# Kernel optimization log

Measured on AMD Instinct MI355X. Metric: run time of the kernel, lower is better.

Reference implementation:

```python
import jax, jax.numpy as jnp
import numpy as np

B, S, HID, NH, NKV, HD, PS = 4, 1024, 4096, 32, 8, 128, 16
PPS = S // PS            # pages per sequence
NP = B * PPS             # total pages
NNZ = B * S


def _llama31_freqs(head_dim):
    # flashinfer apply_llama31_rope defaults: theta=5e5, scale=8, low=1, high=4, old_ctx=8192
    half = head_dim // 2
    theta, scale, low_ff, high_ff, old_ctx = 500000.0, 8.0, 1.0, 4.0, 8192.0
    freq = 1.0 / (theta ** (jnp.arange(half, dtype=jnp.float32) * 2.0 / head_dim))
    wavelen = 2.0 * jnp.pi / freq
    low_wl, high_wl = old_ctx / low_ff, old_ctx / high_ff
    smooth = (old_ctx / wavelen - low_ff) / (high_ff - low_ff)
    return jnp.where(wavelen < high_wl, freq,
                     jnp.where(wavelen > low_wl, freq / scale,
                               (1.0 - smooth) * freq / scale + smooth * freq))


def _rope(x, pos, freqs):
    # x: [nnz, H, D], non-interleaved (rotate-half) layout
    ang = pos.astype(jnp.float32)[:, None] * freqs[None, :]          # [nnz, D/2]
    cos, sin = jnp.cos(ang)[:, None, :], jnp.sin(ang)[:, None, :]    # [nnz, 1, D/2]
    x1, x2 = jnp.split(x, 2, axis=-1)
    return jnp.concatenate([x1 * cos - x2 * sin, x2 * cos + x1 * sin], axis=-1)


def setup_inputs() -> dict:
    key = jax.random.key(0)
    ks = jax.random.split(key, 6)
    std = 0.02
    return {
        "hidden_states": jax.random.normal(ks[0], (NNZ, HID), jnp.float32),
        "wq": jax.random.normal(ks[1], (NH * HD, HID), jnp.float32) * std,
        "wk": jax.random.normal(ks[2], (NKV * HD, HID), jnp.float32) * std,
        "wv": jax.random.normal(ks[3], (NKV * HD, HID), jnp.float32) * std,
        "wo": jax.random.normal(ks[4], (HID, NH * HD), jnp.float32) * std,
        "kv_cache": jnp.zeros((1, NP, 2, PS, NKV, HD), jnp.float32),
        "position_ids": jnp.tile(jnp.arange(S, dtype=jnp.int32), B),
        "kv_page_indices": jnp.arange(NP, dtype=jnp.int32),
        "kv_page_indptr": jnp.arange(B + 1, dtype=jnp.int32) * PPS,
        "kv_last_page_lens": jnp.full((B,), PS, jnp.int32),
        "qo_indptr": jnp.arange(B + 1, dtype=jnp.int32) * S,
    }


def reference(hidden_states, wq, wk, wv, wo, kv_cache, position_ids,
              kv_page_indices, kv_page_indptr, kv_last_page_lens, qo_indptr):
    nnz = hidden_states.shape[0]
    b = qo_indptr.shape[0] - 1
    s = nnz // b
    # fused QKV projections (nn.Linear stores [out, in])
    q = (hidden_states @ wq.T).reshape(nnz, NH, HD)
    k = (hidden_states @ wk.T).reshape(nnz, NKV, HD)
    v = (hidden_states @ wv.T).reshape(nnz, NKV, HD)
    # inline Llama-3.1 RoPE with per-token position ids
    freqs = _llama31_freqs(HD)
    q = _rope(q, position_ids, freqs)
    k = _rope(k, position_ids, freqs)
    # paged-KV append: scatter k/v into pages at (page_id, slot)
    cache = kv_cache[0]                                   # [NP, 2, PS, NKV, HD]
    ps = cache.shape[2]
    pages = kv_page_indices.reshape(b, -1)                # [B, PPS]
    bidx = jnp.repeat(jnp.arange(b), s)
    pid = pages[bidx, position_ids // ps]
    slot = position_ids % ps
    cache = cache.at[pid, 0, slot].set(k).at[pid, 1, slot].set(v)
    # paged attention: gather per-sequence K/V from pages, causal SDPA with GQA
    flat = pages.reshape(-1)
    kf = cache[flat, 0].reshape(b, s, NKV, HD)
    vf = cache[flat, 1].reshape(b, s, NKV, HD)
    g = NH // NKV
    kr = jnp.repeat(kf, g, axis=2)                        # [B, S, NH, HD]
    vr = jnp.repeat(vf, g, axis=2)
    qb = q.reshape(b, s, NH, HD)
    scale = 1.0 / jnp.sqrt(jnp.float32(HD))
    scores = jnp.einsum('bqhd,bkhd->bhqk', qb, kr) * scale
    mask = jnp.tril(jnp.ones((s, s), bool))
    scores = jnp.where(mask[None, None], scores, jnp.float32(-1e30))
    attn = jax.nn.softmax(scores, axis=-1)
    out = jnp.einsum('bhqk,bkhd->bqhd', attn, vr).reshape(nnz, NH * HD)
    return out @ wo.T
```

## Files before the change

kernel.cpp:

```cpp
#include <hip/hip_runtime.h>

typedef unsigned short u16;
typedef __bf16 bf16x8 __attribute__((ext_vector_type(8)));
typedef float f32x4 __attribute__((ext_vector_type(4)));

__device__ __forceinline__ u16 f2bf(float f) {
  unsigned int u = __float_as_uint(f);
  u += 0x7fffu + ((u >> 16) & 1u);
  return (u16)(u >> 16);
}
__device__ __forceinline__ float bf2f(u16 v) {
  return __uint_as_float(((unsigned int)v) << 16);
}

__device__ __forceinline__ void gl_lds16(const u16* g, u16* l) {
  auto* lp = reinterpret_cast<__attribute__((address_space(3))) unsigned int*>(
      reinterpret_cast<uintptr_t>(l));
  auto* gp = reinterpret_cast<const __attribute__((address_space(1))) unsigned int*>(
      reinterpret_cast<uintptr_t>(g));
  __builtin_amdgcn_global_load_lds(gp, lp, 16, 0, 0);
}

__global__ __launch_bounds__(256) void cvt_kernel(const float* __restrict__ in,
                                                  u16* __restrict__ out, int n4) {
  int i = blockIdx.x * 256 + threadIdx.x;
  if (i >= n4) return;
  float4 v = ((const float4*)in)[i];
  ushort4 o;
  o.x = f2bf(v.x); o.y = f2bf(v.y); o.z = f2bf(v.z); o.w = f2bf(v.w);
  ((ushort4*)out)[i] = o;
}


#define BARRIER() __builtin_amdgcn_s_barrier()
#define VMCNT(n_) asm volatile("s_waitcnt vmcnt(" #n_ ")" ::: "memory")
#define PH_SYNC()                                           \
  do {                                                      \
    BARRIER();                                              \
    asm volatile("s_waitcnt lgkmcnt(0)" ::: "memory");      \
    __builtin_amdgcn_sched_barrier(0);                      \
  } while (0)

#define STAGE_A(b_, h_, kt_)                                                        \
  gl_lds16(gA + (size_t)((h_) * 128) * K + (size_t)(kt_) * 32,                      \
           lds + (b_) * 16384 + (h_) * 4096 + w * 512)

#define STAGE_B(b_, h_, kt_)                                                        \
  gl_lds16(gB + (size_t)((h_) * 128) * K + (size_t)(kt_) * 32,                      \
           lds + (b_) * 16384 + 8192 + (h_) * 4096 + w * 512)

#define LOADS_A(b_, qm_)                                                            \
  do {                                                                              \
    _Pragma("unroll") for (int i2 = 0; i2 < 4; i2++)                                \
      ar[i2] = *(const bf16x8*)&lds[(b_) * 16384 + arow + ((qm_)*4 + i2) * 512 + ax]; \
  } while (0)

#define LOADS_B(b_, qn_)                                                            \
  do {                                                                              \
    _Pragma("unroll") for (int j2 = 0; j2 < 2; j2++)                                \
      br[(qn_)*2 + j2] =                                                            \
          *(const bf16x8*)&lds[(b_) * 16384 + brow + ((qn_)*2 + j2) * 512 + ax];    \
  } while (0)

#define MFMA_Q(qm_, qn_)                                                            \
  do {                                                                              \
    __builtin_amdgcn_s_setprio(1);                                                  \
    _Pragma("unroll") for (int i2 = 0; i2 < 4; i2++) {                              \
      _Pragma("unroll") for (int j2 = 0; j2 < 2; j2++) {                            \
        acc[(qm_)*4 + i2][(qn_)*2 + j2] = __builtin_amdgcn_mfma_f32_16x16x32_bf16(  \
            ar[i2], br[(qn_)*2 + j2], acc[(qm_)*4 + i2][(qn_)*2 + j2], 0, 0, 0);    \
      }                                                                             \
    }                                                                               \
    __builtin_amdgcn_s_setprio(0);                                                  \
  } while (0)

template <int OUT_BF16>
__global__ __launch_bounds__(512, 2) void gemm8p(const u16* __restrict__ A,
                                                 const u16* __restrict__ B,
                                                 void* __restrict__ Cv,
                                                 int M, int N, int K) {
  __shared__ u16 lds[32768];
  (void)M;
  const int t = threadIdx.x, lane = t & 63, w = t >> 6;
  const int col = lane & 15, quad = lane >> 4;
  const int wm = w >> 2, wn = w & 3;

  const int nwg = gridDim.x * gridDim.y;
  const int wgid = blockIdx.y * gridDim.x + blockIdx.x;
  const int xcd = wgid & 7, lin = wgid >> 3;
  const int q8 = nwg >> 3, r8 = nwg & 7;
  const int nid = (xcd < r8 ? xcd * (q8 + 1) : r8 * (q8 + 1) + (xcd - r8) * q8) + lin;
  const int m0 = (nid / gridDim.x) * 256;
  const int n0 = (nid % gridDim.x) * 256;

  const int pr_ = t >> 3;
  const int s_ = (t & 7) ^ (pr_ & 7);
  const int srow = (pr_ << 1) | (s_ >> 2);
  const int sj = s_ & 3;
  const u16* gA = A + (size_t)(m0 + srow) * K + sj * 8;
  const u16* gB = B + (size_t)(n0 + srow) * K + sj * 8;

  const int arow = wm * 4096;
  const int brow = 8192 + wn * 2048;
  const int ax = (col >> 1) * 64 +
                 (((((col & 1) << 2) | quad) ^ (col >> 1)) << 3);

  f32x4 acc[8][4] = {};
  bf16x8 ar[4], br[4];

  STAGE_A(0, 0, 0); STAGE_A(0, 1, 0);
  STAGE_B(0, 0, 0); STAGE_B(0, 1, 0);
  STAGE_B(1, 0, 1); STAGE_B(1, 1, 1);
  VMCNT(2);
  BARRIER();

  const int NIT = K >> 6;
  for (int it = 0; it < NIT - 1; ++it) {
    const int kt = it * 2;
    LOADS_A(0, 0); LOADS_B(0, 0);
    STAGE_A(1, 0, kt + 1);
    PH_SYNC(); MFMA_Q(0, 0); BARRIER();
    LOADS_B(0, 1);
    STAGE_A(1, 1, kt + 1);
    PH_SYNC(); MFMA_Q(0, 1); BARRIER();
    LOADS_A(0, 1);
    STAGE_B(0, 0, kt + 2);
    PH_SYNC(); MFMA_Q(1, 0); BARRIER();
    STAGE_B(0, 1, kt + 2);
    PH_SYNC(); MFMA_Q(1, 1); VMCNT(2); BARRIER();
    LOADS_A(1, 0); LOADS_B(1, 0);
    STAGE_A(0, 0, kt + 2);
    PH_SYNC(); MFMA_Q(0, 0); BARRIER();
    LOADS_B(1, 1);
    STAGE_A(0, 1, kt + 2);
    PH_SYNC(); MFMA_Q(0, 1); BARRIER();
    LOADS_A(1, 1);
    STAGE_B(1, 0, kt + 3);
    PH_SYNC(); MFMA_Q(1, 0); BARRIER();
    STAGE_B(1, 1, kt + 3);
    PH_SYNC(); MFMA_Q(1, 1); VMCNT(2); BARRIER();
  }

  {
    const int kl = 2 * NIT - 1;
    LOADS_A(0, 0); LOADS_B(0, 0);
    STAGE_A(1, 0, kl);
    PH_SYNC(); MFMA_Q(0, 0); BARRIER();
    LOADS_B(0, 1);
    STAGE_A(1, 1, kl);
    PH_SYNC(); MFMA_Q(0, 1); BARRIER();
    LOADS_A(0, 1);
    PH_SYNC(); MFMA_Q(1, 0); BARRIER();
    PH_SYNC(); MFMA_Q(1, 1); VMCNT(0); BARRIER();
    LOADS_A(1, 0); LOADS_B(1, 0);
    PH_SYNC(); MFMA_Q(0, 0); BARRIER();
    LOADS_B(1, 1);
    PH_SYNC(); MFMA_Q(0, 1); BARRIER();
    LOADS_A(1, 1);
    PH_SYNC(); MFMA_Q(1, 0); BARRIER();
    MFMA_Q(1, 1);
  }

#pragma unroll
  for (int i = 0; i < 8; i++) {
#pragma unroll
    for (int j = 0; j < 4; j++) {
      const int mb = m0 + wm * 128 + i * 16 + quad * 4;
      const int n = n0 + wn * 64 + j * 16 + col;
#pragma unroll
      for (int r = 0; r < 4; r++) {
        float v = acc[i][j][r];
        if constexpr (OUT_BF16)
          ((u16*)Cv)[(size_t)(mb + r) * N + n] = f2bf(v);
        else
          ((float*)Cv)[(size_t)(mb + r) * N + n] = v;
      }
    }
  }
}

__global__ __launch_bounds__(256) void transpose_kernel(const u16* __restrict__ in,
                                                        u16* __restrict__ out,
                                                        int in_stride, int out_stride) {
  __shared__ u16 tile[64][72];
  const int t = threadIdx.x;
  const int bm = blockIdx.y;
  const int bn = blockIdx.x;
  const int r = t >> 3, c = (t & 7) * 8;
  const u16* src = in + (size_t)(bm * 64 + r) * in_stride + bn * 64 + c;
  *(uint4*)&tile[r][c] = *(const uint4*)src;
  *(uint4*)&tile[r + 32][c] = *(const uint4*)(src + (size_t)32 * in_stride);
  __syncthreads();
  u16 vals[8];
  u16* dst = out + (size_t)(bn * 64 + r) * out_stride + bm * 64 + c;
#pragma unroll
  for (int i = 0; i < 8; i++) vals[i] = tile[c + i][r];
  *(uint4*)dst = *(uint4*)vals;
#pragma unroll
  for (int i = 0; i < 8; i++) vals[i] = tile[c + i][r + 32];
  *(uint4*)(dst + (size_t)32 * out_stride) = *(uint4*)vals;
}

__global__ __launch_bounds__(256) void rope_kernel(u16* __restrict__ X,
                                                   const int* __restrict__ pos_ids,
                                                   int log2H, int row_stride) {
  int tid = blockIdx.x * 256 + threadIdx.x;
  int i = tid & 63;
  int rest = tid >> 6;
  int h = rest & ((1 << log2H) - 1);
  int token = rest >> log2H;
  float pos = (float)pos_ids[token];
  float fr = __builtin_exp2f(-(float)i * (18.93156856932417f / 64.0f));
  float wl = 6.283185307179586f / fr;
  float f2;
  if (wl < 2048.0f) f2 = fr;
  else if (wl > 8192.0f) f2 = fr * 0.125f;
  else {
    float sm = (8192.0f / wl - 1.0f) * (1.0f / 3.0f);
    f2 = (1.0f - sm) * fr * 0.125f + sm * fr;
  }
  float ang = pos * f2;
  float ss = sinf(ang), cc = cosf(ang);
  size_t base = (size_t)token * row_stride + (size_t)h * 128 + i;
  float x1 = bf2f(X[base]), x2 = bf2f(X[base + 64]);
  X[base] = f2bf(x1 * cc - x2 * ss);
  X[base + 64] = f2bf(x2 * cc + x1 * ss);
}

__global__ __launch_bounds__(256) void attn_kernel(const u16* __restrict__ Qg,
                                                   const u16* __restrict__ Kg,
                                                   const u16* __restrict__ VTg,
                                                   u16* __restrict__ Og,
                                                   int QS, int KS) {
  const int qt = 15 - blockIdx.x;
  const int h = blockIdx.y, b = blockIdx.z;
  const int kvh = h >> 2;
  const int t = threadIdx.x, lane = t & 63, w = t >> 6;
  const int col = lane & 15, quad = lane >> 4;

  __shared__ u16 Ks[64 * 128];
  __shared__ u16 Vt[128 * 64];
  __shared__ u16 Ps[4][16][72];

  {
    const u16* Qbase = Qg + (size_t)(b * 1024 + qt * 64) * QS + h * 128;
#pragma unroll
    for (int c = 0; c < 4; c++) {
      int ch = w * 4 + c;
      int row = ch * 4 + (lane >> 4);
      int g = (lane & 15) ^ (row & 15);
      gl_lds16(Qbase + (size_t)row * QS + g * 8, Ks + ch * 512);
    }
  }
  __syncthreads();
  bf16x8 qa[4];
#pragma unroll
  for (int kk = 0; kk < 4; kk++) {
    int row = w * 16 + col;
    qa[kk] = *(const bf16x8*)&Ks[row * 128 + (((quad + 4 * kk) ^ col) << 3)];
  }

  f32x4 o[8] = {};
  float m_i[4] = {-3.0e38f, -3.0e38f, -3.0e38f, -3.0e38f};
  float l_i[4] = {};

  const float cf = 0.08838834764831845f * 1.4426950408889634f;
  const int qrow0 = qt * 64 + w * 16 + quad * 4;

  const u16* Kbase = Kg + (size_t)(b * 1024) * KS + kvh * 128;
  const u16* Vbase = VTg + (size_t)(kvh * 128) * 4096 + b * 1024;

  for (int j = 0; j <= qt; j++) {
    __syncthreads();
#pragma unroll
    for (int c = 0; c < 4; c++) {
      int ch = w * 4 + c;
      int krow = ch * 4 + (lane >> 4);
      int kg = (lane & 15) ^ (krow & 15);
      gl_lds16(Kbase + (size_t)(j * 64 + krow) * KS + kg * 8, Ks + ch * 512);
      int vrow = ch * 8 + (lane >> 3);
      int vg = (lane & 7) ^ (vrow & 7);
      gl_lds16(Vbase + (size_t)vrow * 4096 + j * 64 + vg * 8, Vt + ch * 512);
    }
    __syncthreads();

    f32x4 s[4] = {};
#pragma unroll
    for (int nb = 0; nb < 4; nb++) {
      int key = nb * 16 + col;
#pragma unroll
      for (int kk = 0; kk < 4; kk++) {
        bf16x8 kb2 = *(const bf16x8*)&Ks[key * 128 + (((quad + 4 * kk) ^ col) << 3)];
        s[nb] = __builtin_amdgcn_mfma_f32_16x16x32_bf16(qa[kk], kb2, s[nb], 0, 0, 0);
      }
    }

    if (j == qt) {
#pragma unroll
      for (int nb = 0; nb < 4; nb++)
#pragma unroll
        for (int rr = 0; rr < 4; rr++)
          if (j * 64 + nb * 16 + col > qrow0 + rr) s[nb][rr] = -3.0e38f;
    }

    float mnew[4];
#pragma unroll
    for (int rr = 0; rr < 4; rr++) {
      mnew[rr] = m_i[rr];
#pragma unroll
      for (int nb = 0; nb < 4; nb++) mnew[rr] = fmaxf(mnew[rr], s[nb][rr]);
    }
#pragma unroll
    for (int off = 1; off < 16; off <<= 1)
#pragma unroll
      for (int rr = 0; rr < 4; rr++)
        mnew[rr] = fmaxf(mnew[rr], __shfl_xor(mnew[rr], off));

    float p[4][4], rs[4], alpha[4];
#pragma unroll
    for (int rr = 0; rr < 4; rr++) {
      alpha[rr] = __builtin_exp2f((m_i[rr] - mnew[rr]) * cf);
      m_i[rr] = mnew[rr];
      rs[rr] = 0.0f;
    }
#pragma unroll
    for (int nb = 0; nb < 4; nb++)
#pragma unroll
      for (int rr = 0; rr < 4; rr++) {
        p[nb][rr] = __builtin_exp2f((s[nb][rr] - mnew[rr]) * cf);
        rs[rr] += p[nb][rr];
      }
#pragma unroll
    for (int off = 1; off < 16; off <<= 1)
#pragma unroll
      for (int rr = 0; rr < 4; rr++) rs[rr] += __shfl_xor(rs[rr], off);
#pragma unroll
    for (int rr = 0; rr < 4; rr++) l_i[rr] = l_i[rr] * alpha[rr] + rs[rr];
#pragma unroll
    for (int nb2 = 0; nb2 < 8; nb2++)
#pragma unroll
      for (int rr = 0; rr < 4; rr++) o[nb2][rr] *= alpha[rr];

#pragma unroll
    for (int nb = 0; nb < 4; nb++)
#pragma unroll
      for (int rr = 0; rr < 4; rr++)
        Ps[w][quad * 4 + rr][nb * 16 + col] = f2bf(p[nb][rr]);

    bf16x8 pa0 = *(const bf16x8*)&Ps[w][col][quad * 8];
    bf16x8 pa1 = *(const bf16x8*)&Ps[w][col][quad * 8 + 32];
#pragma unroll
    for (int nb2 = 0; nb2 < 8; nb2++) {
      int d = nb2 * 16 + col;
      bf16x8 vb0 = *(const bf16x8*)&Vt[d * 64 + ((quad ^ (col & 7)) << 3)];
      bf16x8 vb1 = *(const bf16x8*)&Vt[d * 64 + ((((quad + 4) & 7) ^ (col & 7)) << 3)];
      o[nb2] = __builtin_amdgcn_mfma_f32_16x16x32_bf16(pa0, vb0, o[nb2], 0, 0, 0);
      o[nb2] = __builtin_amdgcn_mfma_f32_16x16x32_bf16(pa1, vb1, o[nb2], 0, 0, 0);
    }
  }

  float inv[4];
#pragma unroll
  for (int rr = 0; rr < 4; rr++) inv[rr] = 1.0f / l_i[rr];
#pragma unroll
  for (int nb2 = 0; nb2 < 8; nb2++)
#pragma unroll
    for (int rr = 0; rr < 4; rr++) {
      size_t off2 = (size_t)(b * 1024 + qt * 64 + w * 16 + quad * 4 + rr) * 4096 +
                    h * 128 + nb2 * 16 + col;
      Og[off2] = f2bf(o[nb2][rr] * inv[rr]);
    }
}

extern "C" void kernel_launch(void* const* d_in, const int* in_sizes, int n_in,
                              void* d_out, int out_size, void* d_ws, size_t ws_size,
                              hipStream_t stream) {
  const float* hs = (const float*)d_in[0];
  const float* wq = (const float*)d_in[1];
  const float* wk = (const float*)d_in[2];
  const float* wv = (const float*)d_in[3];
  const float* wo = (const float*)d_in[4];
  const int* pos = (const int*)d_in[6];
  float* out = (float*)d_out;

  char* ws = (char*)d_ws;
  const size_t MB = 1ull << 20;
  u16* hs_bf   = (u16*)(ws + 0);
  u16* wqkv_bf = (u16*)(ws + 32 * MB);
  u16* QKV     = (u16*)(ws + 80 * MB);
  u16* wo_bf = (u16*)(ws + 0);
  u16* AOb   = (u16*)(ws + 32 * MB);
  u16* VTb   = (u16*)(ws + 64 * MB);

  cvt_kernel<<<16384, 256, 0, stream>>>(hs, hs_bf, 4194304);
  cvt_kernel<<<16384, 256, 0, stream>>>(wq, wqkv_bf, 4194304);
  cvt_kernel<<<4096, 256, 0, stream>>>(wk, wqkv_bf + 16777216, 1048576);
  cvt_kernel<<<4096, 256, 0, stream>>>(wv, wqkv_bf + 20971520, 1048576);

  gemm8p<1><<<dim3(24, 16), 512, 0, stream>>>(hs_bf, wqkv_bf, QKV, 4096, 6144, 4096);

  rope_kernel<<<32768, 256, 0, stream>>>(QKV, pos, 5, 6144);
  rope_kernel<<<8192, 256, 0, stream>>>(QKV + 4096, pos, 3, 6144);

  transpose_kernel<<<dim3(16, 64), 256, 0, stream>>>(QKV + 5120, VTb, 6144, 4096);

  cvt_kernel<<<16384, 256, 0, stream>>>(wo, wo_bf, 4194304);

  attn_kernel<<<dim3(16, 32, 4), 256, 0, stream>>>(QKV, QKV + 4096, VTb, AOb, 6144, 6144);

  gemm8p<0><<<dim3(16, 16), 512, 0, stream>>>(AOb, wo_bf, out, 4096, 4096, 4096);
}
```

Baseline: 810.9 us.

## Double-buffer K/V tiles in attention kernel with async prefetch

The attention kernel now keeps two LDS buffers for K and V tiles and issues the global-to-LDS loads for tile j+1 before computing on tile j. It waits on partial vmcnt instead of full barriers. This is meant to hide global memory latency behind the MFMA work. It also raises wave priority around the MFMA blocks. The cost is double the LDS for K/V, about 64KB plus Ps, which may lower occupancy. The BARRIER/VMCNT macros are presumably defined in the unseen part of the file.

Result: no change. 801.4 us (-1.2%).

```diff
diff --git a/kernel.cpp b/kernel.cpp
--- a/kernel.cpp
+++ b/kernel.cpp
@@ -238,9 +238,25 @@
   const int t = threadIdx.x, lane = t & 63, w = t >> 6;
   const int col = lane & 15, quad = lane >> 4;
 
-  __shared__ u16 Ks[64 * 128];
-  __shared__ u16 Vt[128 * 64];
+  __shared__ u16 Ks[2][64 * 128];
+  __shared__ u16 Vt[2][128 * 64];
   __shared__ u16 Ps[4][16][72];
+
+  const u16* Kbase = Kg + (size_t)(b * 1024) * KS + kvh * 128;
+  const u16* Vbase = VTg + (size_t)(kvh * 128) * 4096 + b * 1024;
+
+  auto stage_kv = [&](int bb, int j) {
+#pragma unroll
+    for (int c = 0; c < 4; c++) {
+      int ch = w * 4 + c;
+      int krow = ch * 4 + (lane >> 4);
+      int kg = (lane & 15) ^ (krow & 15);
+      gl_lds16(Kbase + (size_t)(j * 64 + krow) * KS + kg * 8, &Ks[bb][ch * 512]);
+      int vrow = ch * 8 + (lane >> 3);
+      int vg = (lane & 7) ^ (vrow & 7);
+      gl_lds16(Vbase + (size_t)vrow * 4096 + j * 64 + vg * 8, &Vt[bb][ch * 512]);
+    }
+  };
 
   {
     const u16* Qbase = Qg + (size_t)(b * 1024 + qt * 64) * QS + h * 128;
@@ -249,16 +265,18 @@
       int ch = w * 4 + c;
       int row = ch * 4 + (lane >> 4);
       int g = (lane & 15) ^ (row & 15);
-      gl_lds16(Qbase + (size_t)row * QS + g * 8, Ks + ch * 512);
-    }
-  }
+      gl_lds16(Qbase + (size_t)row * QS + g * 8, &Ks[0][ch * 512]);
+    }
+  }
+  stage_kv(1, 0);
   __syncthreads();
   bf16x8 qa[4];
 #pragma unroll
   for (int kk = 0; kk < 4; kk++) {
     int row = w * 16 + col;
-    qa[kk] = *(const bf16x8*)&Ks[row * 128 + (((quad + 4 * kk) ^ col) << 3)];
-  }
+    qa[kk] = *(const bf16x8*)&Ks[0][row * 128 + (((quad + 4 * kk) ^ col) << 3)];
+  }
+  BARRIER();
 
   f32x4 o[8] = {};
   float m_i[4] = {-3.0e38f, -3.0e38f, -3.0e38f, -3.0e38f};
@@ -267,33 +285,31 @@
   const float cf = 0.08838834764831845f * 1.4426950408889634f;
   const int qrow0 = qt * 64 + w * 16 + quad * 4;
 
-  const u16* Kbase = Kg + (size_t)(b * 1024) * KS + kvh * 128;
-  const u16* Vbase = VTg + (size_t)(kvh * 128) * 4096 + b * 1024;
-
   for (int j = 0; j <= qt; j++) {
-    __syncthreads();
-#pragma unroll
-    for (int c = 0; c < 4; c++) {
-      int ch = w * 4 + c;
-      int krow = ch * 4 + (lane >> 4);
-      int kg = (lane & 15) ^ (krow & 15);
-      gl_lds16(Kbase + (size_t)(j * 64 + krow) * KS + kg * 8, Ks + ch * 512);
-      int vrow = ch * 8 + (lane >> 3);
-      int vg = (lane & 7) ^ (vrow & 7);
-      gl_lds16(Vbase + (size_t)vrow * 4096 + j * 64 + vg * 8, Vt + ch * 512);
-    }
-    __syncthreads();
+    const int bb = (j + 1) & 1;
+    if (j < qt) {
+      stage_kv(bb ^ 1, j + 1);
+      VMCNT(8);
+    } else {
+      VMCNT(0);
+    }
+    BARRIER();
+
+    const u16* Ksb = &Ks[bb][0];
+    const u16* Vtb = &Vt[bb][0];
 
     f32x4 s[4] = {};
+    __builtin_amdgcn_s_setprio(1);
 #pragma unroll
     for (int nb = 0; nb < 4; nb++) {
       int key = nb * 16 + col;
 #pragma unroll
       for (int kk = 0; kk < 4; kk++) {
-        bf16x8 kb2 = *(const bf16x8*)&Ks[key * 128 + (((quad + 4 * kk) ^ col) << 3)];
+        bf16x8 kb2 = *(const bf16x8*)&Ksb[key * 128 + (((quad + 4 * kk) ^ col) << 3)];
         s[nb] = __builtin_amdgcn_mfma_f32_16x16x32_bf16(qa[kk], kb2, s[nb], 0, 0, 0);
       }
     }
+    __builtin_amdgcn_s_setprio(0);
 
     if (j == qt) {
 #pragma unroll
@@ -349,14 +365,18 @@
 
     bf16x8 pa0 = *(const bf16x8*)&Ps[w][col][quad * 8];
     bf16x8 pa1 = *(const bf16x8*)&Ps[w][col][quad * 8 + 32];
+    __builtin_amdgcn_s_setprio(1);
 #pragma unroll
     for (int nb2 = 0; nb2 < 8; nb2++) {
       int d = nb2 * 16 + col;
-      bf16x8 vb0 = *(const bf16x8*)&Vt[d * 64 + ((quad ^ (col & 7)) << 3)];
-      bf16x8 vb1 = *(const bf16x8*)&Vt[d * 64 + ((((quad + 4) & 7) ^ (col & 7)) << 3)];
+      bf16x8 vb0 = *(const bf16x8*)&Vtb[d * 64 + ((quad ^ (col & 7)) << 3)];
+      bf16x8 vb1 = *(const bf16x8*)&Vtb[d * 64 + ((((quad + 4) & 7) ^ (col & 7)) << 3)];
       o[nb2] = __builtin_amdgcn_mfma_f32_16x16x32_bf16(pa0, vb0, o[nb2], 0, 0, 0);
       o[nb2] = __builtin_amdgcn_mfma_f32_16x16x32_bf16(pa1, vb1, o[nb2], 0, 0, 0);
     }
+    __builtin_amdgcn_s_setprio(0);
+
+    BARRIER();
   }
 
   float inv[4];
```
